# Kernel optimization log

Measured on AMD Instinct MI355X. Metric: run time of the kernel, lower is better.

## Reference

```python
import jax, jax.numpy as jnp
import numpy as np

DIM = 768
HEADS = 12
HEAD_DIM = DIM // HEADS  # 64
THETA = 10000.0
B, S = 2, 2048


def rotate_half(x):
    # pairs-interleaved rotate: (x1, x2) -> (-x2, x1)
    xp = x.reshape(x.shape[:-1] + (-1, 2))
    x1, x2 = xp[..., 0], xp[..., 1]
    return jnp.stack((-x2, x1), axis=-1).reshape(x.shape)


def rope_freqs(seq_len, head_dim, dtype):
    inv = 1.0 / (THETA ** (jnp.arange(0, head_dim, 2, dtype=jnp.float32) / head_dim))
    pos = jnp.arange(seq_len, dtype=jnp.float32)
    f = pos[:, None] * inv[None, :]              # [S, head_dim//2]
    f = jnp.repeat(f, 2, axis=-1)                # [S, head_dim]
    return f.astype(dtype)


def apply_rotary(freqs, t):
    # freqs [S, D] broadcasts against t [B, H, S, D]
    return t * jnp.cos(freqs) + rotate_half(t) * jnp.sin(freqs)


def setup_inputs() -> dict:
    key = jax.random.key(0)
    k1, k2, k3 = jax.random.split(key, 3)
    x = jax.random.normal(k1, (B, S, DIM), dtype=jnp.float32)
    W_qkv = jax.random.normal(k2, (3 * DIM, DIM), dtype=jnp.float32) * 0.02
    W_proj = jax.random.normal(k3, (DIM, DIM), dtype=jnp.float32) * 0.02
    b_proj = jnp.zeros((DIM,), dtype=jnp.float32)
    return {"x": x, "W_qkv": W_qkv, "W_proj": W_proj, "b_proj": b_proj}


def reference(x, W_qkv, W_proj, b_proj):
    Bb, Ss, C = x.shape
    qkv = jnp.einsum('bsc,oc->bso', x, W_qkv)                    # [B,S,3C]
    qkv = qkv.reshape(Bb, Ss, 3, HEADS, HEAD_DIM)
    qkv = jnp.transpose(qkv, (2, 0, 3, 1, 4))                    # [3,B,H,S,D]
    q, k, v = qkv[0], qkv[1], qkv[2]
    freqs = rope_freqs(Ss, HEAD_DIM, x.dtype)
    q = apply_rotary(freqs, q)
    k = apply_rotary(freqs, k)
    scale = HEAD_DIM ** -0.5
    scores = jnp.einsum('bhqd,bhkd->bhqk', q, k) * scale         # [B,H,S,S]
    probs = jax.nn.softmax(scores, axis=-1)
    out = jnp.einsum('bhqk,bhkd->bhqd', probs, v)                # [B,H,S,D]
    out = jnp.transpose(out, (0, 2, 1, 3)).reshape(Bb, Ss, C)
    return jnp.einsum('bsc,oc->bso', out, W_proj) + b_proj
```

## Files before the change

### kernel.cpp

```cpp
#include <hip/hip_runtime.h>
#include <math.h>

#define Bq 2
#define Sq 2048
#define Cq 768
#define Hq 12
#define Dq 64

#define PANEL_SHORTS 98304
#define PANELS_X  32
#define PANELS_WQ 18
#define PANELS_WP 6

typedef _Float16 f16x8 __attribute__((ext_vector_type(8)));
typedef __fp16 fp16v2 __attribute__((ext_vector_type(2)));
typedef float f32x4 __attribute__((ext_vector_type(4)));
#define MFMA16F(a, b, c) __builtin_amdgcn_mfma_f32_16x16x32_f16(a, b, c, 0, 0, 0)

#define SCALEQ 0.18033688011112042f

static __device__ inline unsigned short f16bits(float x) {
    _Float16 h = (_Float16)x;
    return __builtin_bit_cast(unsigned short, h);
}
static __device__ inline unsigned int pk16(float a, float b) {
    fp16v2 h = __builtin_amdgcn_cvt_pkrtz(a, b);
    return __builtin_bit_cast(unsigned int, h);
}

static __device__ inline void gld_lds16(const unsigned short* g, unsigned short* l) {
    __builtin_amdgcn_global_load_lds(
        (const __attribute__((address_space(1))) unsigned int*)g,
        (__attribute__((address_space(3))) unsigned int*)l, 16, 0, 0);
}

__global__ void freq_kernel(float* __restrict__ ctab, float* __restrict__ stab) {
    int idx = blockIdx.x * blockDim.x + threadIdx.x;
    int s = idx >> 5;
    int i = idx & 31;
    double f = (double)s * exp(-(double)i * 0.28782313662425573);
    ctab[idx] = (float)cos(f);
    stab[idx] = (float)sin(f);
}

__global__ __launch_bounds__(256) void split_kernel(
    const float* __restrict__ x, const float* __restrict__ wq,
    const float* __restrict__ wp,
    unsigned short* __restrict__ xs, unsigned short* __restrict__ wqs,
    unsigned short* __restrict__ wps)
{
    const int cid  = blockIdx.x * 256 + threadIdx.x;
    const int panel = cid / 12288;
    const int pos8  = cid % 12288;
    const int step = pos8 >> 10;
    const int rem  = pos8 & 1023;
    const int J    = rem >> 6;
    const int lane = rem & 63;
    const int rowp = J * 8 + (lane >> 3);
    const int lc   = (lane & 7) ^ (rowp & 7);
    const int k    = step * 64 + lc * 8;
    const float* src; unsigned short* dst; int prow;
    if (panel < PANELS_X) {
        src = x;  dst = xs;  prow = panel;
    } else if (panel < PANELS_X + PANELS_WQ) {
        src = wq; dst = wqs; prow = panel - PANELS_X;
    } else {
        src = wp; dst = wps; prow = panel - PANELS_X - PANELS_WQ;
    }
    const int row = prow * 128 + rowp;
    float4 v0 = *(const float4*)(src + (size_t)row * Cq + k);
    float4 v1 = *(const float4*)(src + (size_t)row * Cq + k + 4);
    unsigned short o[8] = { f16bits(v0.x), f16bits(v0.y), f16bits(v0.z),
                            f16bits(v0.w), f16bits(v1.x), f16bits(v1.y),
                            f16bits(v1.z), f16bits(v1.w) };
    *(uint4*)&dst[(size_t)prow * PANEL_SHORTS + (size_t)pos8 * 8] = *(uint4*)o;
}

template <int MODE, int BM, int BN>
__global__ __launch_bounds__(256) void gemm_mfma_kernel(
    const unsigned short* __restrict__ Apr, const unsigned short* __restrict__ Bpr,
    const float* __restrict__ ctab, const float* __restrict__ stab,
    unsigned short* __restrict__ qp, unsigned short* __restrict__ kp,
    unsigned short* __restrict__ vp,
    float* __restrict__ out0, const float* __restrict__ bias)
{
    constexpr int MI  = BM / 32;
    constexpr int NI  = BN / 32;
    constexpr int WTM = BM / 2;
    constexpr int WTN = BN / 2;
    constexpr int BCH = BN / 8;
    constexpr int ACH = BM / 8;
    constexpr int CPW = (ACH + BCH) / 4;

    __shared__ unsigned short sA[BM * 64];
    __shared__ unsigned short sB[BN * 64];

    const int t    = threadIdx.x;
    const int w    = t >> 6;
    const int lane = t & 63;
    const int ml   = lane & 15;
    const int quad = lane >> 4;
    const int wm   = w >> 1;
    const int wn   = w & 1;

    const int mBase = blockIdx.y * BM;
    const int nBase = blockIdx.x * BN;

    const unsigned short* gpanA = Apr + (size_t)(mBase >> 7) * PANEL_SHORTS;
    const unsigned short* gpanB = Bpr + (size_t)(nBase >> 7) * PANEL_SHORTS;
    const int JbA = (mBase & 127) >> 3;
    const int JbB = (nBase & 127) >> 3;

    f32x4 acc[MI][NI];
    #pragma unroll
    for (int mi = 0; mi < MI; ++mi)
        #pragma unroll
        for (int ni = 0; ni < NI; ++ni)
            acc[mi][ni] = (f32x4){0.f, 0.f, 0.f, 0.f};

    for (int k0 = 0; k0 < 12; ++k0) {
        __syncthreads();
        #pragma unroll
        for (int cc = 0; cc < CPW; ++cc) {
            const int c = w * CPW + cc;
            if (c < BCH) {
                gld_lds16(gpanB + k0 * 8192 + (JbB + c) * 512 + lane * 8,
                          sB + c * 512);
            } else {
                const int a = c - BCH;
                gld_lds16(gpanA + k0 * 8192 + (JbA + a) * 512 + lane * 8,
                          sA + a * 512);
            }
        }
        __syncthreads();

        f16x8 aF[MI][2], bF[NI][2];
        #pragma unroll
        for (int mi = 0; mi < MI; ++mi) {
            const int row = wm * WTM + mi * 16 + ml;
            #pragma unroll
            for (int ks = 0; ks < 2; ++ks)
                aF[mi][ks] = *(const f16x8*)
                    &sA[row * 64 + (((ks * 4 + quad) ^ (row & 7)) << 3)];
        }
        #pragma unroll
        for (int ni = 0; ni < NI; ++ni) {
            const int row = wn * WTN + ni * 16 + ml;
            #pragma unroll
            for (int ks = 0; ks < 2; ++ks)
                bF[ni][ks] = *(const f16x8*)
                    &sB[row * 64 + (((ks * 4 + quad) ^ (row & 7)) << 3)];
        }
        #pragma unroll
        for (int mi = 0; mi < MI; ++mi)
            #pragma unroll
            for (int ni = 0; ni < NI; ++ni) {
                acc[mi][ni] = MFMA16F(aF[mi][0], bF[ni][0], acc[mi][ni]);
                acc[mi][ni] = MFMA16F(aF[mi][1], bF[ni][1], acc[mi][ni]);
            }
    }

    if (MODE == 0) {
        const int which = nBase / Cq;
        #pragma unroll
        for (int mi = 0; mi < MI; ++mi) {
            const int gm = mBase + wm * WTM + mi * 16 + quad * 4;
            const int bb = gm >> 11;
            const int s0 = gm & 2047;
            #pragma unroll
            for (int ni = 0; ni < NI; ++ni) {
                const int gn = nBase + wn * WTN + ni * 16 + ml;
                const int c  = gn - which * Cq;
                const int hh = c >> 6;
                const int dd = c & 63;
                const size_t hb = (size_t)(bb * Hq + hh);
                if (which < 2) {
                    #pragma unroll
                    for (int r = 0; r < 4; ++r) {
                        float val = acc[mi][ni][r];
                        float pv  = __shfl_xor(val, 1, 64);
                        const int fi = (s0 + r) * 32 + (dd >> 1);
                        float c0 = ctab[fi], sn = stab[fi];
                        float o = (dd & 1) ? (val * c0 + pv * sn)
                                           : (val * c0 - pv * sn);
                        if (which == 0) {
                            o *= SCALEQ;
                            qp[(hb * Sq + s0 + r) * 64 + dd] = f16bits(o);
                        } else {
                            const int ss = s0 + r, rr = ss & 63, kt2 = ss >> 6;
                            kp[(hb * 32 + kt2) * 4096 + rr * 64
                               + (((dd >> 3) ^ (rr & 7)) << 3) + (dd & 7)] = f16bits(o);
                        }
                    }
                } else {
                    unsigned short hv[4];
                    #pragma unroll
                    for (int r = 0; r < 4; ++r)
                        hv[r] = f16bits(acc[mi][ni][r]);
                    const int kt2 = s0 >> 6;
                    *(ushort4*)&vp[(hb * 32 + kt2) * 4096 + dd * 64
                        + ((((s0 & 63) >> 3) ^ (dd & 7)) << 3) + (s0 & 7)]
                        = *(ushort4*)hv;
                }
            }
        }
    } else {
        #pragma unroll
        for (int mi = 0; mi < MI; ++mi) {
            const int gm = mBase + wm * WTM + mi * 16 + quad * 4;
            #pragma unroll
            for (int ni = 0; ni < NI; ++ni) {
                const int gn = nBase + wn * WTN + ni * 16 + ml;
                const float bz = bias[gn];
                #pragma unroll
                for (int r = 0; r < 4; ++r)
                    out0[(size_t)(gm + r) * Cq + gn] = acc[mi][ni][r] + bz;
            }
        }
    }
}

__global__ __launch_bounds__(256, 3) void attn_mfma_kernel(
    const unsigned short* __restrict__ qp, const unsigned short* __restrict__ kp,
    const unsigned short* __restrict__ vp, unsigned short* __restrict__ attns)
{
    __shared__ __align__(16) unsigned short smem[20480];
    unsigned short* pb = smem + 16384;

    const int t    = threadIdx.x;
    const int w    = t >> 6;
    const int lane = t & 63;
    const int ml   = lane & 15;
    const int quad = lane >> 4;
    const int bi   = blockIdx.x;
    const int bh   = bi % 24;
    const int qt   = bi / 24;

    const bool isV = (w >= 2);
    const unsigned short* gsrc = isV ? vp : kp;
    const int Jb = (w & 1) * 4;
    const size_t gb = (size_t)bh * 131072;
    unsigned short* sMine = smem + (isV ? 8192 : 0);

    auto stage = [&](int buf, int kt) {
        const unsigned short* gt = gsrc + gb + (size_t)kt * 4096;
        unsigned short* sd = sMine + buf * 4096;
        #pragma unroll
        for (int j = 0; j < 4; ++j)
            gld_lds16(gt + (Jb + j) * 512 + lane * 8, sd + (Jb + j) * 512);
    };

    stage(0, 0);

    const size_t qrow = ((size_t)bh * Sq + qt * 64 + w * 16 + ml) * 64;
    f16x8 bQ[2];
    bQ[0] = *(const f16x8*)(qp + qrow + quad * 8);
    bQ[1] = *(const f16x8*)(qp + qrow + 32 + quad * 8);

    float m_st = -INFINITY, l_st = 0.f;
    f32x4 O[4];
    #pragma unroll
    for (int ng = 0; ng < 4; ++ng) O[ng] = (f32x4){0.f, 0.f, 0.f, 0.f};

    unsigned short* pbl = pb + (w * 16 + ml) * 64;
    const int rsw = ml & 7;

    __syncthreads();

    for (int kt = 0; kt < 32; ++kt) {
        const int cur = kt & 1;
        if (kt + 1 < 32) stage(cur ^ 1, kt + 1);
        const unsigned short* k_s = smem + cur * 4096;
        const unsigned short* v_s = smem + 8192 + cur * 4096;

        f32x4 S[4];
        #pragma unroll
        for (int ng = 0; ng < 4; ++ng) {
            const int row = ng * 16 + ml;
            f32x4 acc = (f32x4){0.f, 0.f, 0.f, 0.f};
            #pragma unroll
            for (int ks = 0; ks < 2; ++ks) {
                f16x8 aK = *(const f16x8*)
                    &k_s[row * 64 + (((ks * 4 + quad) ^ (row & 7)) << 3)];
                acc = MFMA16F(aK, bQ[ks], acc);
            }
            S[ng] = acc;
        }

        float a0 = fmaxf(fmaxf(S[0][0], S[0][1]), fmaxf(S[0][2], S[0][3]));
        float a1 = fmaxf(fmaxf(S[1][0], S[1][1]), fmaxf(S[1][2], S[1][3]));
        float a2 = fmaxf(fmaxf(S[2][0], S[2][1]), fmaxf(S[2][2], S[2][3]));
        float a3 = fmaxf(fmaxf(S[3][0], S[3][1]), fmaxf(S[3][2], S[3][3]));
        float mx = fmaxf(fmaxf(a0, a1), fmaxf(a2, a3));
        mx = fmaxf(mx, __shfl_xor(mx, 16, 64));
        mx = fmaxf(mx, __shfl_xor(mx, 32, 64));
        if (__any(mx > m_st + 11.f)) {
            float nm = fmaxf(m_st, mx);
            float al = exp2f(m_st - nm);
            #pragma unroll
            for (int ng = 0; ng < 4; ++ng) O[ng] = O[ng] * al;
            l_st *= al;
            m_st = nm;
        }

        float ps = 0.f;
        #pragma unroll
        for (int ng = 0; ng < 4; ++ng) {
            float p0 = exp2f(S[ng][0] - m_st);
            float p1 = exp2f(S[ng][1] - m_st);
            float p2 = exp2f(S[ng][2] - m_st);
            float p3 = exp2f(S[ng][3] - m_st);
            ps += (p0 + p1) + (p2 + p3);
            uint2 u;
            u.x = pk16(p0, p1);
            u.y = pk16(p2, p3);
            const int ch = ng * 2 + (quad >> 1);
            *(uint2*)&pbl[((ch ^ rsw) << 3) + (quad & 1) * 4] = u;
        }
        ps += __shfl_xor(ps, 16, 64);
        ps += __shfl_xor(ps, 32, 64);
        l_st += ps;

        #pragma unroll
        for (int ks = 0; ks < 2; ++ks) {
            uint4 pu = *(const uint4*)&pbl[(((ks * 4 + quad) ^ rsw) << 3)];
            f16x8 bP = __builtin_bit_cast(f16x8, pu);
            #pragma unroll
            for (int ngd = 0; ngd < 4; ++ngd) {
                const int row = ngd * 16 + ml;
                f16x8 aV = *(const f16x8*)
                    &v_s[row * 64 + (((ks * 4 + quad) ^ (row & 7)) << 3)];
                O[ngd] = MFMA16F(aV, bP, O[ngd]);
            }
        }
        __syncthreads();
    }

    float* obuf = (float*)smem;
    {
        const float il = 1.0f / l_st;
        float* obl = obuf + (w * 16 + ml) * 68;
        #pragma unroll
        for (int ngd = 0; ngd < 4; ++ngd) {
            f32x4 ov = O[ngd] * il;
            *(f32x4*)&obl[ngd * 16 + quad * 4] = ov;
        }
    }
    __syncthreads();
    const int bb = bh / Hq, hh = bh % Hq;
    #pragma unroll
    for (int r = 0; r < 4; ++r) {
        const int srow = qt * 64 + w * 16 + quad * 4 + r;
        const int mrow = bb * 2048 + srow;
        const int panel = mrow >> 7, r128 = mrow & 127;
        const size_t rbase = (size_t)panel * PANEL_SHORTS
                           + (r128 >> 3) * 512 + (r128 & 7) * 64;
        #pragma unroll
        for (int ng = 0; ng < 4; ++ng) {
            const int k = hh * 64 + ng * 16 + ml;
            float o = obuf[(w * 16 + quad * 4 + r) * 68 + ng * 16 + ml];
            const int step = k >> 6;
            const int lc   = (k & 63) >> 3;
            attns[rbase + (size_t)step * 8192
                  + ((lc ^ (r128 & 7)) << 3) + (k & 7)] = f16bits(o);
        }
    }
}

extern "C" void kernel_launch(void* const* d_in, const int* in_sizes, int n_in,
                              void* d_out, int out_size, void* d_ws, size_t ws_size,
                              hipStream_t stream) {
    const float* x     = (const float*)d_in[0];
    const float* Wqkv  = (const float*)d_in[1];
    const float* Wproj = (const float*)d_in[2];
    const float* bproj = (const float*)d_in[3];
    float* out = (float*)d_out;

    char* p = (char*)d_ws;
    unsigned short* xs    = (unsigned short*)p; p += (size_t)PANELS_X  * PANEL_SHORTS * 2;
    unsigned short* wqs   = (unsigned short*)p; p += (size_t)PANELS_WQ * PANEL_SHORTS * 2;
    unsigned short* wps   = (unsigned short*)p; p += (size_t)PANELS_WP * PANEL_SHORTS * 2;
    unsigned short* qp    = (unsigned short*)p; p += (size_t)24 * Sq * 64 * 2;
    unsigned short* kp    = (unsigned short*)p; p += (size_t)24 * 131072 * 2;
    unsigned short* vp    = (unsigned short*)p; p += (size_t)24 * 131072 * 2;
    unsigned short* attns = (unsigned short*)p; p += (size_t)PANELS_X * PANEL_SHORTS * 2;
    float* ctab = (float*)p; p += (size_t)Sq * 32 * 4;
    float* stab = (float*)p; p += (size_t)Sq * 32 * 4;

    freq_kernel<<<256, 256, 0, stream>>>(ctab, stab);
    split_kernel<<<(PANELS_X + PANELS_WQ + PANELS_WP) * 12288 / 256, 256, 0, stream>>>(
        x, Wqkv, Wproj, xs, wqs, wps);
    gemm_mfma_kernel<0, 64, 128><<<dim3(18, 64), 256, 0, stream>>>(
        xs, wqs, ctab, stab, qp, kp, vp, nullptr, nullptr);
    attn_mfma_kernel<<<dim3(32 * 24), 256, 0, stream>>>(qp, kp, vp, attns);
    gemm_mfma_kernel<1, 64, 64><<<dim3(12, 64), 256, 0, stream>>>(
        attns, wps, ctab, stab, nullptr, nullptr, nullptr, out, bproj);
}
```

Baseline: 181.7 us.

## Split attention KV range in halves and merge with a combine kernel

Each attention block now processes only half of the key/value tiles, writing normalized fp16 partial outputs plus per-row max and sum to workspace. A new combine kernel rescales and merges the two halves into the swizzled panel layout consumed by the projection GEMM. LDS double buffering is removed in favour of a single synchronously loaded tile, allowing higher occupancy (launch bound 6). This trades extra global traffic, an additional launch and lost load/compute overlap for more parallelism and resident blocks.

```diff
diff --git a/kernel.cpp b/kernel.cpp
--- a/kernel.cpp
+++ b/kernel.cpp
@@ -11,6 +11,9 @@
 #define PANELS_X  32
 #define PANELS_WQ 18
 #define PANELS_WP 6
+
+#define NROWS 49152
+#define OPHALF 3145728
 
 typedef _Float16 f16x8 __attribute__((ext_vector_type(8)));
 typedef __fp16 fp16v2 __attribute__((ext_vector_type(2)));
@@ -220,12 +223,13 @@
     }
 }
 
-__global__ __launch_bounds__(256, 3) void attn_mfma_kernel(
+__global__ __launch_bounds__(256, 6) void attn_mfma_kernel(
     const unsigned short* __restrict__ qp, const unsigned short* __restrict__ kp,
-    const unsigned short* __restrict__ vp, unsigned short* __restrict__ attns)
+    const unsigned short* __restrict__ vp, unsigned short* __restrict__ op,
+    float2* __restrict__ mlp)
 {
-    __shared__ __align__(16) unsigned short smem[20480];
-    unsigned short* pb = smem + 16384;
+    __shared__ __align__(16) unsigned short smem[12288];
+    unsigned short* pb = smem + 8192;
 
     const int t    = threadIdx.x;
     const int w    = t >> 6;
@@ -234,23 +238,15 @@
     const int quad = lane >> 4;
     const int bi   = blockIdx.x;
     const int bh   = bi % 24;
-    const int qt   = bi / 24;
+    const int rest = bi / 24;
+    const int qt   = rest >> 1;
+    const int half = rest & 1;
 
     const bool isV = (w >= 2);
     const unsigned short* gsrc = isV ? vp : kp;
     const int Jb = (w & 1) * 4;
     const size_t gb = (size_t)bh * 131072;
-    unsigned short* sMine = smem + (isV ? 8192 : 0);
-
-    auto stage = [&](int buf, int kt) {
-        const unsigned short* gt = gsrc + gb + (size_t)kt * 4096;
-        unsigned short* sd = sMine + buf * 4096;
-        #pragma unroll
-        for (int j = 0; j < 4; ++j)
-            gld_lds16(gt + (Jb + j) * 512 + lane * 8, sd + (Jb + j) * 512);
-    };
-
-    stage(0, 0);
+    unsigned short* sdst = smem + (isV ? 4096 : 0);
 
     const size_t qrow = ((size_t)bh * Sq + qt * 64 + w * 16 + ml) * 64;
     f16x8 bQ[2];
@@ -265,13 +261,19 @@
     unsigned short* pbl = pb + (w * 16 + ml) * 64;
     const int rsw = ml & 7;
 
-    __syncthreads();
-
-    for (int kt = 0; kt < 32; ++kt) {
-        const int cur = kt & 1;
-        if (kt + 1 < 32) stage(cur ^ 1, kt + 1);
-        const unsigned short* k_s = smem + cur * 4096;
-        const unsigned short* v_s = smem + 8192 + cur * 4096;
+    const unsigned short* k_s = smem;
+    const unsigned short* v_s = smem + 4096;
+
+    for (int kt16 = 0; kt16 < 16; ++kt16) {
+        const int kt = half * 16 + kt16;
+        __syncthreads();
+        {
+            const unsigned short* gt = gsrc + gb + (size_t)kt * 4096;
+            #pragma unroll
+            for (int j = 0; j < 4; ++j)
+                gld_lds16(gt + (Jb + j) * 512 + lane * 8, sdst + (Jb + j) * 512);
+        }
+        __syncthreads();
 
         f32x4 S[4];
         #pragma unroll
@@ -333,38 +335,55 @@
                 O[ngd] = MFMA16F(aV, bP, O[ngd]);
             }
         }
-        __syncthreads();
     }
 
-    float* obuf = (float*)smem;
-    {
-        const float il = 1.0f / l_st;
-        float* obl = obuf + (w * 16 + ml) * 68;
-        #pragma unroll
-        for (int ngd = 0; ngd < 4; ++ngd) {
-            f32x4 ov = O[ngd] * il;
-            *(f32x4*)&obl[ngd * 16 + quad * 4] = ov;
-        }
+    const int srow = qt * 64 + w * 16 + ml;
+    const size_t rowb = (size_t)half * NROWS + (size_t)bh * 2048 + srow;
+    if (quad == 0) mlp[rowb] = make_float2(m_st, l_st);
+    const float il = 1.0f / l_st;
+    #pragma unroll
+    for (int ngd = 0; ngd < 4; ++ngd) {
+        unsigned short o4[4];
+        #pragma unroll
+        for (int r = 0; r < 4; ++r)
+            o4[r] = f16bits(O[ngd][r] * il);
+        *(ushort4*)&op[rowb * 64 + ngd * 16 + quad * 4] = *(ushort4*)o4;
     }
-    __syncthreads();
+}
+
+__global__ __launch_bounds__(256) void combine_kernel(
+    const unsigned short* __restrict__ op, const float2* __restrict__ mlp,
+    unsigned short* __restrict__ attns)
+{
+    const int g   = blockIdx.x * 256 + threadIdx.x;
+    const int row = g >> 3;
+    const int ch  = g & 7;
+    const int bh  = row >> 11;
+    const int s   = row & 2047;
+
+    const float2 ml1 = mlp[row];
+    const float2 ml2 = mlp[NROWS + row];
+    const float M  = fmaxf(ml1.x, ml2.x);
+    const float a1 = ml1.y * exp2f(ml1.x - M);
+    const float a2 = ml2.y * exp2f(ml2.x - M);
+    const float inv = 1.0f / (a1 + a2);
+    const float c1 = a1 * inv, c2 = a2 * inv;
+
+    f16x8 h1 = *(const f16x8*)(op + (size_t)row * 64 + ch * 8);
+    f16x8 h2 = *(const f16x8*)(op + OPHALF + (size_t)row * 64 + ch * 8);
+    unsigned short o[8];
+    #pragma unroll
+    for (int j = 0; j < 8; ++j)
+        o[j] = f16bits(c1 * (float)h1[j] + c2 * (float)h2[j]);
+
     const int bb = bh / Hq, hh = bh % Hq;
-    #pragma unroll
-    for (int r = 0; r < 4; ++r) {
-        const int srow = qt * 64 + w * 16 + quad * 4 + r;
-        const int mrow = bb * 2048 + srow;
-        const int panel = mrow >> 7, r128 = mrow & 127;
-        const size_t rbase = (size_t)panel * PANEL_SHORTS
-                           + (r128 >> 3) * 512 + (r128 & 7) * 64;
-        #pragma unroll
-        for (int ng = 0; ng < 4; ++ng) {
-            const int k = hh * 64 + ng * 16 + ml;
-            float o = obuf[(w * 16 + quad * 4 + r) * 68 + ng * 16 + ml];
-            const int step = k >> 6;
-            const int lc   = (k & 63) >> 3;
-            attns[rbase + (size_t)step * 8192
-                  + ((lc ^ (r128 & 7)) << 3) + (k & 7)] = f16bits(o);
-        }
-    }
+    const int mrow = bb * 2048 + s;
+    const int panel = mrow >> 7, r128 = mrow & 127;
+    const size_t addr = (size_t)panel * PANEL_SHORTS
+                      + (r128 >> 3) * 512 + (r128 & 7) * 64
+                      + (size_t)hh * 8192
+                      + ((ch ^ (r128 & 7)) << 3);
+    *(uint4*)&attns[addr] = *(uint4*)o;
 }
 
 extern "C" void kernel_launch(void* const* d_in, const int* in_sizes, int n_in,
@@ -384,6 +403,8 @@
     unsigned short* kp    = (unsigned short*)p; p += (size_t)24 * 131072 * 2;
     unsigned short* vp    = (unsigned short*)p; p += (size_t)24 * 131072 * 2;
     unsigned short* attns = (unsigned short*)p; p += (size_t)PANELS_X * PANEL_SHORTS * 2;
+    unsigned short* op    = (unsigned short*)p; p += (size_t)2 * OPHALF * 2;
+    float2* mlp           = (float2*)p;         p += (size_t)2 * NROWS * 8;
     float* ctab = (float*)p; p += (size_t)Sq * 32 * 4;
     float* stab = (float*)p; p += (size_t)Sq * 32 * 4;
 
@@ -392,7 +413,8 @@
         x, Wqkv, Wproj, xs, wqs, wps);
     gemm_mfma_kernel<0, 64, 128><<<dim3(18, 64), 256, 0, stream>>>(
         xs, wqs, ctab, stab, qp, kp, vp, nullptr, nullptr);
-    attn_mfma_kernel<<<dim3(32 * 24), 256, 0, stream>>>(qp, kp, vp, attns);
+    attn_mfma_kernel<<<dim3(24 * 64), 256, 0, stream>>>(qp, kp, vp, op, mlp);
+    combine_kernel<<<dim3(1536), 256, 0, stream>>>(op, mlp, attns);
     gemm_mfma_kernel<1, 64, 64><<<dim3(12, 64), 256, 0, stream>>>(
         attns, wps, ctab, stab, nullptr, nullptr, nullptr, out, bproj);
 }
```

Result: no change. 183.5 us (+1.0%).
